# Kernel optimization log

Hardware: AMD Instinct MI355X
Metric: run time of the kernel (lower is better)

Reference implementation:

```python
import jax, jax.numpy as jnp
import numpy as np

# ---- module config (matches init_kwargs) ----
M_CTRL, N_CTRL = 64, 64      # control grid
P_DEG, Q_DEG = 3, 3          # degrees
OUT = 512                    # evaluation grid per axis
DIM = 3                      # spatial dimension (homogeneous = DIM+1)
BATCH = 16


def gen_knot_vector(p, n):
    num_segments = (p + n + 1) - 2 * (p + 1) + 1
    return np.array([0.0] * p + list(np.linspace(0.0, 1.0, num_segments)) + [1.0] * p,
                    dtype=np.float64)


def find_span(n_ctrl, p, u, U):
    # NURBS Book A2.1
    n = n_ctrl - 1
    if u >= U[n + 1]:
        return n
    if u <= U[p]:
        return p
    low, high = p, n + 1
    mid = (low + high) // 2
    while u < U[mid] or u >= U[mid + 1]:
        if u < U[mid]:
            high = mid
        else:
            low = mid
        mid = (low + high) // 2
    return mid


def basis_funs(span, u, p, U):
    # NURBS Book A2.2 -> (p+1,) nonzero basis values
    Nb = np.zeros(p + 1)
    Nb[0] = 1.0
    left = np.zeros(p + 1)
    right = np.zeros(p + 1)
    for j in range(1, p + 1):
        left[j] = u - U[span + 1 - j]
        right[j] = U[span + j] - u
        saved = 0.0
        for r in range(j):
            temp = Nb[r] / (right[r + 1] + left[j - r])
            Nb[r] = saved + right[r + 1] * temp
            saved = left[j - r] * temp
        Nb[j] = saved
    return Nb


def precompute_basis(params, p, n_ctrl):
    U = gen_knot_vector(p, n_ctrl)
    spans = np.array([find_span(n_ctrl, p, float(u), U) for u in params], dtype=np.int32)
    Nb = np.stack([basis_funs(int(s), float(u), p, U) for s, u in zip(spans, params)])
    return jnp.asarray(spans), jnp.asarray(Nb.astype(np.float32))


def setup_inputs() -> dict:
    key = jax.random.key(0)
    k1, k2 = jax.random.split(key)
    xyz = jax.random.normal(k1, (BATCH, M_CTRL, N_CTRL, DIM), dtype=jnp.float32)
    # positive weights keep the rational division well-conditioned
    w = jax.random.uniform(k2, (BATCH, M_CTRL, N_CTRL, 1), dtype=jnp.float32,
                           minval=0.5, maxval=1.5)
    ctrl_pts = jnp.concatenate([xyz, w], axis=-1)  # homogeneous [B, m, n, DIM+1]

    u = np.linspace(0.0, 0.99, OUT)
    v = np.linspace(0.0, 0.99, OUT)
    uspan, Nu = precompute_basis(u, P_DEG, M_CTRL)  # [OUT], [OUT, p+1]
    vspan, Nv = precompute_basis(v, Q_DEG, N_CTRL)  # [OUT], [OUT, q+1]
    return {"ctrl_pts": ctrl_pts, "uspan": uspan, "vspan": vspan, "Nu": Nu, "Nv": Nv}


def reference(ctrl_pts, uspan, vspan, Nu, Nv):
    p = Nu.shape[1] - 1
    q = Nv.shape[1] - 1
    # local control-point index windows
    idx_u = uspan[:, None] - p + jnp.arange(p + 1)[None, :]   # [OUT, p+1]
    idx_v = vspan[:, None] - q + jnp.arange(q + 1)[None, :]   # [OUT, q+1]
    # contract u-basis first: gather [B, OUT, p+1, n, c] -> [B, OUT, n, c]
    pts_u = ctrl_pts[:, idx_u, :, :]
    A = jnp.einsum('ur,burnc->bunc', Nu, pts_u)
    # then v: gather [B, OUT, OUT, q+1, c] -> homogeneous surface [B, OUT, OUT, c]
    pts_v = A[:, :, idx_v, :]
    Sw = jnp.einsum('vs,buvsc->buvc', Nv, pts_v)
    # rational division
    return Sw[..., :DIM] / Sw[..., DIM:DIM + 1]
```

## Files before the change

kernel.cpp:

```cpp
#include <hip/hip_runtime.h>

#define OUTN 512
#define NCTL 64
#define BATCH 16

__global__ __launch_bounds__(256) void surfeval_kernel(
    const float* __restrict__ ctrl,
    const int*   __restrict__ uspan,
    const int*   __restrict__ vspan,
    const float* __restrict__ Nu,
    const float* __restrict__ Nv,
    float*       __restrict__ out)
{
    __shared__ float A[NCTL][4];

    const int u = blockIdx.x;
    const int b = blockIdx.y;
    const int t = threadIdx.x;

    const int v0 = t;
    const int v1 = t + 256;
    const int sv0 = vspan[v0];
    const int sv1 = vspan[v1];
    const float4 nv0 = ((const float4*)Nv)[v0];
    const float4 nv1 = ((const float4*)Nv)[v1];

    const int su = uspan[u];
    const float4 nu = ((const float4*)Nu)[u];
    {
        const float* p = ctrl + ((size_t)b * NCTL + (size_t)(su - 3)) * (NCTL * 4) + t;
        A[t >> 2][t & 3] = nu.x * p[0]
                         + nu.y * p[NCTL * 4]
                         + nu.z * p[2 * NCTL * 4]
                         + nu.w * p[3 * NCTL * 4];
    }
    __syncthreads();

    float* __restrict__ orow = out + ((size_t)b * OUTN + (size_t)u) * (OUTN * 3);

    {
        const float4* Af = (const float4*)(&A[sv0 - 3][0]);
        const float4 s0 = Af[0], s1 = Af[1], s2 = Af[2], s3 = Af[3];
        const float sx = nv0.x * s0.x + nv0.y * s1.x + nv0.z * s2.x + nv0.w * s3.x;
        const float sy = nv0.x * s0.y + nv0.y * s1.y + nv0.z * s2.y + nv0.w * s3.y;
        const float sz = nv0.x * s0.z + nv0.y * s1.z + nv0.z * s2.z + nv0.w * s3.z;
        const float sw = nv0.x * s0.w + nv0.y * s1.w + nv0.z * s2.w + nv0.w * s3.w;
        const float inv = 1.0f / sw;
        orow[v0 * 3 + 0] = sx * inv;
        orow[v0 * 3 + 1] = sy * inv;
        orow[v0 * 3 + 2] = sz * inv;
    }
    {
        const float4* Af = (const float4*)(&A[sv1 - 3][0]);
        const float4 s0 = Af[0], s1 = Af[1], s2 = Af[2], s3 = Af[3];
        const float sx = nv1.x * s0.x + nv1.y * s1.x + nv1.z * s2.x + nv1.w * s3.x;
        const float sy = nv1.x * s0.y + nv1.y * s1.y + nv1.z * s2.y + nv1.w * s3.y;
        const float sz = nv1.x * s0.z + nv1.y * s1.z + nv1.z * s2.z + nv1.w * s3.z;
        const float sw = nv1.x * s0.w + nv1.y * s1.w + nv1.z * s2.w + nv1.w * s3.w;
        const float inv = 1.0f / sw;
        orow[v1 * 3 + 0] = sx * inv;
        orow[v1 * 3 + 1] = sy * inv;
        orow[v1 * 3 + 2] = sz * inv;
    }
}

extern "C" void kernel_launch(void* const* d_in, const int* in_sizes, int n_in,
                              void* d_out, int out_size, void* d_ws, size_t ws_size,
                              hipStream_t stream) {
    const float* ctrl  = (const float*)d_in[0];
    const int*   uspan = (const int*)d_in[1];
    const int*   vspan = (const int*)d_in[2];
    const float* Nu    = (const float*)d_in[3];
    const float* Nv    = (const float*)d_in[4];
    float* out = (float*)d_out;

    dim3 grid(OUTN, BATCH);
    surfeval_kernel<<<grid, 256, 0, stream>>>(ctrl, uspan, vspan, Nu, Nv, out);
}
```

Before: 80.75 us.

## Stage outputs in LDS for float4 stores and use per-wave A rows

Each wave now computes its own copy of the u-contracted row using float4 loads, which removes the block-wide __syncthreads in favour of wave barriers. Each thread evaluates two adjacent v points. Results go to a per-wave LDS buffer and are written to global memory as coalesced float4 stores instead of strided scalar stores. The cost is fourfold redundant row computation and extra shared memory.

```diff
diff --git a/kernel.cpp b/kernel.cpp
--- a/kernel.cpp
+++ b/kernel.cpp
@@ -12,14 +12,17 @@
     const float* __restrict__ Nv,
     float*       __restrict__ out)
 {
-    __shared__ float A[NCTL][4];
+    __shared__ float A[4][NCTL][4];
+    __shared__ float S[4][128 * 3];
 
     const int u = blockIdx.x;
     const int b = blockIdx.y;
     const int t = threadIdx.x;
+    const int w = t >> 6;
+    const int l = t & 63;
 
-    const int v0 = t;
-    const int v1 = t + 256;
+    const int v0 = 2 * t;
+    const int v1 = v0 + 1;
     const int sv0 = vspan[v0];
     const int sv1 = vspan[v1];
     const float4 nv0 = ((const float4*)Nv)[v0];
@@ -27,40 +30,55 @@
 
     const int su = uspan[u];
     const float4 nu = ((const float4*)Nu)[u];
-    {
-        const float* p = ctrl + ((size_t)b * NCTL + (size_t)(su - 3)) * (NCTL * 4) + t;
-        A[t >> 2][t & 3] = nu.x * p[0]
-                         + nu.y * p[NCTL * 4]
-                         + nu.z * p[2 * NCTL * 4]
-                         + nu.w * p[3 * NCTL * 4];
-    }
-    __syncthreads();
-
-    float* __restrict__ orow = out + ((size_t)b * OUTN + (size_t)u) * (OUTN * 3);
 
     {
-        const float4* Af = (const float4*)(&A[sv0 - 3][0]);
+        const float4* crow =
+            (const float4*)(ctrl + ((size_t)b * NCTL + (size_t)(su - 3)) * (NCTL * 4)) + l;
+        const float4 r0 = crow[0];
+        const float4 r1 = crow[NCTL];
+        const float4 r2 = crow[2 * NCTL];
+        const float4 r3 = crow[3 * NCTL];
+        float4 a;
+        a.x = nu.x * r0.x + nu.y * r1.x + nu.z * r2.x + nu.w * r3.x;
+        a.y = nu.x * r0.y + nu.y * r1.y + nu.z * r2.y + nu.w * r3.y;
+        a.z = nu.x * r0.z + nu.y * r1.z + nu.z * r2.z + nu.w * r3.z;
+        a.w = nu.x * r0.w + nu.y * r1.w + nu.z * r2.w + nu.w * r3.w;
+        ((float4*)A[w])[l] = a;
+    }
+    __builtin_amdgcn_wave_barrier();
+
+    {
+        const float4* Af = (const float4*)(&A[w][sv0 - 3][0]);
         const float4 s0 = Af[0], s1 = Af[1], s2 = Af[2], s3 = Af[3];
         const float sx = nv0.x * s0.x + nv0.y * s1.x + nv0.z * s2.x + nv0.w * s3.x;
         const float sy = nv0.x * s0.y + nv0.y * s1.y + nv0.z * s2.y + nv0.w * s3.y;
         const float sz = nv0.x * s0.z + nv0.y * s1.z + nv0.z * s2.z + nv0.w * s3.z;
         const float sw = nv0.x * s0.w + nv0.y * s1.w + nv0.z * s2.w + nv0.w * s3.w;
         const float inv = 1.0f / sw;
-        orow[v0 * 3 + 0] = sx * inv;
-        orow[v0 * 3 + 1] = sy * inv;
-        orow[v0 * 3 + 2] = sz * inv;
+        S[w][l * 6 + 0] = sx * inv;
+        S[w][l * 6 + 1] = sy * inv;
+        S[w][l * 6 + 2] = sz * inv;
     }
     {
-        const float4* Af = (const float4*)(&A[sv1 - 3][0]);
+        const float4* Af = (const float4*)(&A[w][sv1 - 3][0]);
         const float4 s0 = Af[0], s1 = Af[1], s2 = Af[2], s3 = Af[3];
         const float sx = nv1.x * s0.x + nv1.y * s1.x + nv1.z * s2.x + nv1.w * s3.x;
         const float sy = nv1.x * s0.y + nv1.y * s1.y + nv1.z * s2.y + nv1.w * s3.y;
         const float sz = nv1.x * s0.z + nv1.y * s1.z + nv1.z * s2.z + nv1.w * s3.z;
         const float sw = nv1.x * s0.w + nv1.y * s1.w + nv1.z * s2.w + nv1.w * s3.w;
         const float inv = 1.0f / sw;
-        orow[v1 * 3 + 0] = sx * inv;
-        orow[v1 * 3 + 1] = sy * inv;
-        orow[v1 * 3 + 2] = sz * inv;
+        S[w][l * 6 + 3] = sx * inv;
+        S[w][l * 6 + 4] = sy * inv;
+        S[w][l * 6 + 5] = sz * inv;
+    }
+    __builtin_amdgcn_wave_barrier();
+
+    {
+        float* orow = out + ((size_t)b * OUTN + (size_t)u) * (OUTN * 3);
+        float4* og = (float4*)orow + 96 * w;
+        const float4* sg = (const float4*)S[w];
+        og[l] = sg[l];
+        if (l < 32) og[64 + l] = sg[64 + l];
     }
 }
 
```

Measured after the change: 82.57 us. 1.02x slower.
